# Kernel tuning notes

Hardware: AMD Instinct MI355X
Metric: run time of the kernel (lower is better)

## Reference

```python
import jax, jax.numpy as jnp
import numpy as np


def setup_inputs() -> dict:
    key = jax.random.key(0)
    k1, k2 = jax.random.split(key)
    B, N, M, C = 32, 4096, 4096, 3
    xyz1 = jax.random.normal(k1, (B, N, C), dtype=jnp.float32)
    xyz2 = jax.random.normal(k2, (B, M, C), dtype=jnp.float32)
    return {"xyz1": xyz1, "xyz2": xyz2}


def _chamfer_l2(xyz1, xyz2):
    # Pairwise squared L2 distances via ||a||^2 + ||b||^2 - 2 a.b  (b n m)
    sq1 = jnp.sum(xyz1 * xyz1, axis=-1)            # [B, N]
    sq2 = jnp.sum(xyz2 * xyz2, axis=-1)            # [B, M]
    cross = jnp.einsum('bnc,bmc->bnm', xyz1, xyz2) # [B, N, M]
    d = sq1[:, :, None] + sq2[:, None, :] - 2.0 * cross
    dist1 = jnp.min(d, axis=2)                     # [B, N] nearest in xyz2
    dist2 = jnp.min(d, axis=1)                     # [B, M] nearest in xyz1
    return jnp.mean(dist1, axis=-1) + jnp.mean(dist2, axis=-1)  # [B]


def reference(xyz1, xyz2):
    return _chamfer_l2(xyz1, xyz2)
```

## Files before the change

kernel.cpp:

```cpp
#include <hip/hip_runtime.h>

typedef _Float16 half8 __attribute__((ext_vector_type(8)));
typedef float floatx16 __attribute__((ext_vector_type(16)));

#define TPB   256
#define RPTS  1024
#define NTILE (RPTS / 32)
#define SMH   (RPTS * 16)

__device__ __forceinline__ unsigned enc(float f) {
    int b = __float_as_int(f);
    return (b >= 0) ? ((unsigned)b | 0x80000000u) : ~(unsigned)b;
}
__device__ __forceinline__ float dec(unsigned k) {
    int b = (k & 0x80000000u) ? (int)(k & 0x7FFFFFFFu) : (int)~k;
    return __int_as_float(b);
}

__global__ __launch_bounds__(256) void pack_frags(const float* __restrict__ src,
                                                  _Float16* __restrict__ dst,
                                                  int npts, int npad) {
    const int b = blockIdx.y;
    const int p = blockIdx.x * 256 + (int)threadIdx.x;
    if (p >= npad) return;
    const int g = p < npts ? p : npts - 1;
    const float* sp = src + ((size_t)b * npts + g) * 3;
    float x = sp[0], y = sp[1], z = sp[2];
    float hq = 0.5f * (x * x + y * y + z * z);
    _Float16 xh = (_Float16)x, yh = (_Float16)y, zh = (_Float16)z;
    _Float16 xl = (_Float16)(x - (float)xh);
    _Float16 yl = (_Float16)(y - (float)yh);
    _Float16 zl = (_Float16)(z - (float)zh);
    _Float16 qh = (_Float16)hq;
    _Float16 ql = (_Float16)(hq - (float)qh);
    const _Float16 hz = (_Float16)0.0f;
    half8 v0, v1;
    v0[0] = xh; v0[1] = xl; v0[2] = xh; v0[3] = yh;
    v0[4] = yl; v0[5] = yh; v0[6] = zh; v0[7] = zl;
    v1[0] = zh; v1[1] = qh; v1[2] = ql; v1[3] = hz;
    v1[4] = hz; v1[5] = hz; v1[6] = hz; v1[7] = hz;
    int t = p >> 5, c = p & 31;
    _Float16* base = dst + (size_t)b * npad * 16 + (size_t)t * 512 + c * 8;
    *(half8*)base         = v0;
    *(half8*)(base + 256) = v1;
}

__global__ __launch_bounds__(TPB, 4) void chamfer_ws(const float* __restrict__ xyz1,
                                                     const float* __restrict__ xyz2,
                                                     const _Float16* __restrict__ frag1,
                                                     const _Float16* __restrict__ frag2,
                                                     unsigned* __restrict__ dist,
                                                     int N, int M, int B,
                                                     int p1pad, int p2pad, int qpad) {
    const int b = blockIdx.y, dir = blockIdx.z;
    const float*    __restrict__ P = dir ? xyz2 + (size_t)b * M * 3 : xyz1 + (size_t)b * N * 3;
    const _Float16* __restrict__ F = dir ? frag1 + (size_t)b * p1pad * 16
                                         : frag2 + (size_t)b * p2pad * 16;
    const int nq    = dir ? M : N;
    const int mdpad = dir ? p1pad : p2pad;

    const int qblk = blockIdx.x >> 1;
    const int s    = blockIdx.x & 1;
    if (qblk * 256 >= nq) return;

    __shared__ __align__(16) _Float16 smB[SMH];

    const int tid = (int)threadIdx.x;
    const int w   = tid >> 6;
    const int l   = tid & 63;
    const int m   = l & 31;
    const int h   = l >> 5;

    const _Float16 hz = (_Float16)0.0f, hone = (_Float16)1.0f;
    const int qb = qblk * 256 + w * 64;

    half8 afr[2];
#pragma unroll
    for (int g = 0; g < 2; ++g) {
        int idx = qb + g * 32 + m;
        int ci  = idx < nq ? idx : nq - 1;
        float x = P[3 * ci], y = P[3 * ci + 1], z = P[3 * ci + 2];
        _Float16 xh = (_Float16)x, yh = (_Float16)y, zh = (_Float16)z;
        _Float16 xl = (_Float16)(x - (float)xh);
        _Float16 yl = (_Float16)(y - (float)yh);
        _Float16 zl = (_Float16)(z - (float)zh);
        half8 a;
        if (h == 0) {
            a[0] = -xh; a[1] = -xh; a[2] = -xl; a[3] = -yh;
            a[4] = -yh; a[5] = -yl; a[6] = -zh; a[7] = -zh;
        } else {
            a[0] = -zl; a[1] = hone; a[2] = hone; a[3] = hz;
            a[4] = hz;  a[5] = hz;   a[6] = hz;  a[7] = hz;
        }
        afr[g] = a;
    }

    float rm[32];
#pragma unroll
    for (int i = 0; i < 32; ++i) rm[i] = 3.0e38f;

    const floatx16 czero = {0.0f, 0.0f, 0.0f, 0.0f, 0.0f, 0.0f, 0.0f, 0.0f,
                            0.0f, 0.0f, 0.0f, 0.0f, 0.0f, 0.0f, 0.0f, 0.0f};
    const int nrounds = mdpad / RPTS;
    const _Float16* bp = smB + h * 256 + m * 8;

    for (int r = s; r < nrounds; r += 2) {
        if (r != s) __syncthreads();
        const int4* __restrict__ gsrc = (const int4*)(F + (size_t)r * SMH);
        int4* __restrict__ ldst = (int4*)smB;
#pragma unroll
        for (int k = 0; k < (SMH * 2 / 16) / TPB; ++k) {
            int c = k * TPB + tid;
            ldst[c] = gsrc[c];
        }
        __syncthreads();

        for (int t = 0; t < NTILE; t += 2) {
            half8 b0 = *(const half8*)(bp + t * 512);
            half8 b1 = *(const half8*)(bp + t * 512 + 512);
            floatx16 d0a = __builtin_amdgcn_mfma_f32_32x32x16_f16(afr[0], b0, czero, 0, 0, 0);
            floatx16 d0b = __builtin_amdgcn_mfma_f32_32x32x16_f16(afr[0], b1, czero, 0, 0, 0);
#pragma unroll
            for (int i = 0; i < 16; ++i)
                rm[i] = fminf(fminf(rm[i], d0a[i]), d0b[i]);
            floatx16 d1a = __builtin_amdgcn_mfma_f32_32x32x16_f16(afr[1], b0, czero, 0, 0, 0);
            floatx16 d1b = __builtin_amdgcn_mfma_f32_32x32x16_f16(afr[1], b1, czero, 0, 0, 0);
#pragma unroll
            for (int i = 0; i < 16; ++i)
                rm[16 + i] = fminf(fminf(rm[16 + i], d1a[i]), d1b[i]);
        }
    }

#pragma unroll
    for (int off = 1; off < 32; off <<= 1) {
#pragma unroll
        for (int i = 0; i < 32; ++i) rm[i] = fminf(rm[i], __shfl_xor(rm[i], off, 64));
    }

    unsigned* dptr = dist + (size_t)(dir * B + b) * qpad;
    if (m < 16) {
        const int reg = (m & 3) + 4 * (m >> 2);
        const int row = 4 * h + (m & 3) + 8 * (m >> 2);
#pragma unroll
        for (int g = 0; g < 2; ++g) {
            int idx = qb + g * 32 + row;
            if (idx < nq) {
                float x = P[3 * idx], y = P[3 * idx + 1], z = P[3 * idx + 2];
                float v = rm[g * 16 + reg] + 0.5f * (x * x + y * y + z * z);
                atomicMin(dptr + idx, enc(v));
            }
        }
    }
}

__global__ __launch_bounds__(256) void reduce_out(const unsigned* __restrict__ dist,
                                                  float* __restrict__ out,
                                                  int N, int M, int B, int qpad) {
    const int b = blockIdx.x;
    const int tid = (int)threadIdx.x;
    float s = 0.0f;
    const unsigned* d0 = dist + (size_t)b * qpad;
    const unsigned* d1 = dist + (size_t)(B + b) * qpad;
    for (int i = tid; i < N; i += 256) s += dec(d0[i]) * (1.0f / (float)N);
    for (int i = tid; i < M; i += 256) s += dec(d1[i]) * (1.0f / (float)M);
#pragma unroll
    for (int off = 32; off > 0; off >>= 1) s += __shfl_down(s, off, 64);
    __shared__ float red[4];
    if ((tid & 63) == 0) red[tid >> 6] = s;
    __syncthreads();
    if (tid == 0) out[b] = 2.0f * (red[0] + red[1] + red[2] + red[3]);
}

__global__ __launch_bounds__(TPB, 4) void chamfer_plain(const float* __restrict__ xyz1,
                                                        const float* __restrict__ xyz2,
                                                        float* __restrict__ out,
                                                        int N, int M) {
    const int b = blockIdx.y, dir = blockIdx.z;
    const float* __restrict__ P = dir ? xyz2 + (size_t)b * M * 3 : xyz1 + (size_t)b * N * 3;
    const float* __restrict__ Q = dir ? xyz1 + (size_t)b * N * 3 : xyz2 + (size_t)b * M * 3;
    const int nq = dir ? M : N;
    const int md = dir ? N : M;
    if ((int)blockIdx.x * TPB >= nq) return;
    __shared__ __align__(16) _Float16 smB[SMH];
    const int tid = (int)threadIdx.x;
    const int w = tid >> 6, l = tid & 63, m = l & 31, h = l >> 5;
    const _Float16 hz = (_Float16)0.0f, hone = (_Float16)1.0f;
    const int qb = blockIdx.x * 256 + w * 64;
    half8 afr[2];
#pragma unroll
    for (int g = 0; g < 2; ++g) {
        int idx = qb + g * 32 + m;
        int ci  = idx < nq ? idx : nq - 1;
        float x = P[3 * ci], y = P[3 * ci + 1], z = P[3 * ci + 2];
        _Float16 xh = (_Float16)x, yh = (_Float16)y, zh = (_Float16)z;
        _Float16 xl = (_Float16)(x - (float)xh);
        _Float16 yl = (_Float16)(y - (float)yh);
        _Float16 zl = (_Float16)(z - (float)zh);
        half8 a;
        if (h == 0) { a[0]=-xh;a[1]=-xh;a[2]=-xl;a[3]=-yh;a[4]=-yh;a[5]=-yl;a[6]=-zh;a[7]=-zh; }
        else        { a[0]=-zl;a[1]=hone;a[2]=hone;a[3]=hz;a[4]=hz;a[5]=hz;a[6]=hz;a[7]=hz; }
        afr[g] = a;
    }
    float rm[32];
#pragma unroll
    for (int i = 0; i < 32; ++i) rm[i] = 3.0e38f;
    const floatx16 czero = {0,0,0,0,0,0,0,0,0,0,0,0,0,0,0,0};
    const int nrounds = (md + RPTS - 1) / RPTS;
    const _Float16* bp = smB + h * 256 + m * 8;
    for (int r = 0; r < nrounds; ++r) {
        if (r) __syncthreads();
#pragma unroll
        for (int k = 0; k < RPTS / TPB; ++k) {
            int j = tid + k * TPB;
            int g = r * RPTS + j;
            g = g < md ? g : md - 1;
            float x = Q[3 * g], y = Q[3 * g + 1], z = Q[3 * g + 2];
            float hq = 0.5f * (x * x + y * y + z * z);
            _Float16 xh = (_Float16)x, yh = (_Float16)y, zh = (_Float16)z;
            _Float16 xl = (_Float16)(x - (float)xh);
            _Float16 yl = (_Float16)(y - (float)yh);
            _Float16 zl = (_Float16)(z - (float)zh);
            _Float16 qh = (_Float16)hq;
            _Float16 ql = (_Float16)(hq - (float)qh);
            int t = j >> 5, c = j & 31;
            half8 v0, v1;
            v0[0]=xh;v0[1]=xl;v0[2]=xh;v0[3]=yh;v0[4]=yl;v0[5]=yh;v0[6]=zh;v0[7]=zl;
            v1[0]=zh;v1[1]=qh;v1[2]=ql;v1[3]=hz;v1[4]=hz;v1[5]=hz;v1[6]=hz;v1[7]=hz;
            *(half8*)&smB[t * 512 + c * 8]       = v0;
            *(half8*)&smB[t * 512 + 256 + c * 8] = v1;
        }
        __syncthreads();
        for (int t = 0; t < NTILE; t += 2) {
            half8 b0 = *(const half8*)(bp + t * 512);
            half8 b1 = *(const half8*)(bp + t * 512 + 512);
            floatx16 d0a = __builtin_amdgcn_mfma_f32_32x32x16_f16(afr[0], b0, czero, 0, 0, 0);
            floatx16 d0b = __builtin_amdgcn_mfma_f32_32x32x16_f16(afr[0], b1, czero, 0, 0, 0);
#pragma unroll
            for (int i = 0; i < 16; ++i) rm[i] = fminf(fminf(rm[i], d0a[i]), d0b[i]);
            floatx16 d1a = __builtin_amdgcn_mfma_f32_32x32x16_f16(afr[1], b0, czero, 0, 0, 0);
            floatx16 d1b = __builtin_amdgcn_mfma_f32_32x32x16_f16(afr[1], b1, czero, 0, 0, 0);
#pragma unroll
            for (int i = 0; i < 16; ++i) rm[16+i] = fminf(fminf(rm[16+i], d1a[i]), d1b[i]);
        }
    }
#pragma unroll
    for (int off = 1; off < 32; off <<= 1) {
#pragma unroll
        for (int i = 0; i < 32; ++i) rm[i] = fminf(rm[i], __shfl_xor(rm[i], off, 64));
    }
    float s = 0.0f;
    if (m < 16) {
        const int reg = (m & 3) + 4 * (m >> 2);
        const int row = 4 * h + (m & 3) + 8 * (m >> 2);
#pragma unroll
        for (int g = 0; g < 2; ++g) {
            int idx = qb + g * 32 + row;
            if (idx < nq) {
                float x = P[3 * idx], y = P[3 * idx + 1], z = P[3 * idx + 2];
                s += rm[g * 16 + reg] + 0.5f * (x * x + y * y + z * z);
            }
        }
    }
#pragma unroll
    for (int off = 32; off > 0; off >>= 1) s += __shfl_down(s, off, 64);
    if (l == 0) atomicAdd(out + b, s * (2.0f / (float)nq));
}

extern "C" void kernel_launch(void* const* d_in, const int* in_sizes, int n_in,
                              void* d_out, int out_size, void* d_ws, size_t ws_size,
                              hipStream_t stream) {
    const float* xyz1 = (const float*)d_in[0];
    const float* xyz2 = (const float*)d_in[1];
    float* out = (float*)d_out;

    const int B = out_size;
    const int N = in_sizes[0] / (3 * B);
    const int M = in_sizes[1] / (3 * B);
    const int qmax = N > M ? N : M;

    const int p1pad = ((N + RPTS - 1) / RPTS) * RPTS;
    const int p2pad = ((M + RPTS - 1) / RPTS) * RPTS;
    const int qpad  = p1pad > p2pad ? p1pad : p2pad;
    const size_t f1bytes = (size_t)B * p1pad * 32;
    const size_t f2bytes = (size_t)B * p2pad * 32;
    const size_t dbytes  = (size_t)2 * B * qpad * sizeof(unsigned);

    if (ws_size >= f1bytes + f2bytes + dbytes) {
        _Float16* frag1 = (_Float16*)d_ws;
        _Float16* frag2 = (_Float16*)((char*)d_ws + f1bytes);
        unsigned* dist  = (unsigned*)((char*)d_ws + f1bytes + f2bytes);

        pack_frags<<<dim3(p1pad / 256, B), dim3(256), 0, stream>>>(xyz1, frag1, N, p1pad);
        pack_frags<<<dim3(p2pad / 256, B), dim3(256), 0, stream>>>(xyz2, frag2, M, p2pad);
        hipMemsetAsync(dist, 0xFF, dbytes, stream);

        dim3 grid(((qmax + 255) / 256) * 2, B, 2);
        chamfer_ws<<<grid, dim3(TPB), 0, stream>>>(xyz1, xyz2, frag1, frag2, dist,
                                                   N, M, B, p1pad, p2pad, qpad);
        reduce_out<<<dim3(B), dim3(256), 0, stream>>>(dist, out, N, M, B, qpad);
    } else {
        hipMemsetAsync(out, 0, (size_t)B * sizeof(float), stream);
        dim3 grid((qmax + 255) / 256, B, 2);
        chamfer_plain<<<grid, dim3(TPB), 0, stream>>>(xyz1, xyz2, out, N, M);
    }
}
```

Baseline: 117.9 us.

## Fuse pack/memset launches, split query work four ways, software-pipeline MFMA min loop

Merges the two pack kernels and the distance memset into one launch that also zeros the output, removing several launch overheads. Raises the work split over reference rounds from 2 to 4 blocks per query tile, giving more blocks and parallelism but more atomic-min traffic and fewer rounds per block. Software-pipelines the MFMA loop so the next tile's matrix products are issued before the previous results are min-reduced, hiding MFMA latency at the cost of extra registers. The final reduce now accumulates into the output instead of overwriting it.

```diff
diff --git a/kernel.cpp b/kernel.cpp
--- a/kernel.cpp
+++ b/kernel.cpp
@@ -7,6 +7,7 @@
 #define RPTS  1024
 #define NTILE (RPTS / 32)
 #define SMH   (RPTS * 16)
+#define SPLIT 4
 
 __device__ __forceinline__ unsigned enc(float f) {
     int b = __float_as_int(f);
@@ -17,20 +18,37 @@
     return __int_as_float(b);
 }
 
-__global__ __launch_bounds__(256) void pack_frags(const float* __restrict__ src,
-                                                  _Float16* __restrict__ dst,
-                                                  int npts, int npad) {
+__global__ __launch_bounds__(256) void pack_all(const float* __restrict__ xyz1,
+                                                const float* __restrict__ xyz2,
+                                                _Float16* __restrict__ frag1,
+                                                _Float16* __restrict__ frag2,
+                                                unsigned* __restrict__ dist,
+                                                float* __restrict__ out,
+                                                int N, int M, int B,
+                                                int p1pad, int p2pad, int qpad) {
     const int b = blockIdx.y;
+    const int z = blockIdx.z;
     const int p = blockIdx.x * 256 + (int)threadIdx.x;
+
+    if (z == 0 && b == 0 && blockIdx.x == 0) {
+        for (int i = (int)threadIdx.x; i < B; i += 256) out[i] = 0.0f;
+    }
+    if (p < qpad) dist[(size_t)(z * B + b) * qpad + p] = 0xFFFFFFFFu;
+
+    const int   npts = z ? M : N;
+    const int   npad = z ? p2pad : p1pad;
     if (p >= npad) return;
+    const float* src = z ? xyz2 : xyz1;
+    _Float16*    dst = z ? frag2 : frag1;
+
     const int g = p < npts ? p : npts - 1;
     const float* sp = src + ((size_t)b * npts + g) * 3;
-    float x = sp[0], y = sp[1], z = sp[2];
-    float hq = 0.5f * (x * x + y * y + z * z);
-    _Float16 xh = (_Float16)x, yh = (_Float16)y, zh = (_Float16)z;
+    float x = sp[0], y = sp[1], zc = sp[2];
+    float hq = 0.5f * (x * x + y * y + zc * zc);
+    _Float16 xh = (_Float16)x, yh = (_Float16)y, zh = (_Float16)zc;
     _Float16 xl = (_Float16)(x - (float)xh);
     _Float16 yl = (_Float16)(y - (float)yh);
-    _Float16 zl = (_Float16)(z - (float)zh);
+    _Float16 zl = (_Float16)(zc - (float)zh);
     _Float16 qh = (_Float16)hq;
     _Float16 ql = (_Float16)(hq - (float)qh);
     const _Float16 hz = (_Float16)0.0f;
@@ -59,8 +77,8 @@
     const int nq    = dir ? M : N;
     const int mdpad = dir ? p1pad : p2pad;
 
-    const int qblk = blockIdx.x >> 1;
-    const int s    = blockIdx.x & 1;
+    const int qblk = blockIdx.x / SPLIT;
+    const int s    = blockIdx.x % SPLIT;
     if (qblk * 256 >= nq) return;
 
     __shared__ __align__(16) _Float16 smB[SMH];
@@ -104,7 +122,7 @@
     const int nrounds = mdpad / RPTS;
     const _Float16* bp = smB + h * 256 + m * 8;
 
-    for (int r = s; r < nrounds; r += 2) {
+    for (int r = s; r < nrounds; r += SPLIT) {
         if (r != s) __syncthreads();
         const int4* __restrict__ gsrc = (const int4*)(F + (size_t)r * SMH);
         int4* __restrict__ ldst = (int4*)smB;
@@ -115,19 +133,30 @@
         }
         __syncthreads();
 
-        for (int t = 0; t < NTILE; t += 2) {
-            half8 b0 = *(const half8*)(bp + t * 512);
-            half8 b1 = *(const half8*)(bp + t * 512 + 512);
-            floatx16 d0a = __builtin_amdgcn_mfma_f32_32x32x16_f16(afr[0], b0, czero, 0, 0, 0);
-            floatx16 d0b = __builtin_amdgcn_mfma_f32_32x32x16_f16(afr[0], b1, czero, 0, 0, 0);
-#pragma unroll
-            for (int i = 0; i < 16; ++i)
-                rm[i] = fminf(fminf(rm[i], d0a[i]), d0b[i]);
-            floatx16 d1a = __builtin_amdgcn_mfma_f32_32x32x16_f16(afr[1], b0, czero, 0, 0, 0);
-            floatx16 d1b = __builtin_amdgcn_mfma_f32_32x32x16_f16(afr[1], b1, czero, 0, 0, 0);
-#pragma unroll
-            for (int i = 0; i < 16; ++i)
-                rm[16 + i] = fminf(fminf(rm[16 + i], d1a[i]), d1b[i]);
+        half8 c0 = *(const half8*)(bp);
+        half8 c1 = *(const half8*)(bp + 512);
+        floatx16 p0a = __builtin_amdgcn_mfma_f32_32x32x16_f16(afr[0], c0, czero, 0, 0, 0);
+        floatx16 p0b = __builtin_amdgcn_mfma_f32_32x32x16_f16(afr[0], c1, czero, 0, 0, 0);
+        floatx16 p1a = __builtin_amdgcn_mfma_f32_32x32x16_f16(afr[1], c0, czero, 0, 0, 0);
+        floatx16 p1b = __builtin_amdgcn_mfma_f32_32x32x16_f16(afr[1], c1, czero, 0, 0, 0);
+        for (int t = 2; t < NTILE; t += 2) {
+            half8 n0 = *(const half8*)(bp + t * 512);
+            half8 n1 = *(const half8*)(bp + t * 512 + 512);
+            floatx16 q0a = __builtin_amdgcn_mfma_f32_32x32x16_f16(afr[0], n0, czero, 0, 0, 0);
+            floatx16 q0b = __builtin_amdgcn_mfma_f32_32x32x16_f16(afr[0], n1, czero, 0, 0, 0);
+            floatx16 q1a = __builtin_amdgcn_mfma_f32_32x32x16_f16(afr[1], n0, czero, 0, 0, 0);
+            floatx16 q1b = __builtin_amdgcn_mfma_f32_32x32x16_f16(afr[1], n1, czero, 0, 0, 0);
+#pragma unroll
+            for (int i = 0; i < 16; ++i) {
+                rm[i]      = fminf(fminf(rm[i],      p0a[i]), p0b[i]);
+                rm[16 + i] = fminf(fminf(rm[16 + i], p1a[i]), p1b[i]);
+            }
+            p0a = q0a; p0b = q0b; p1a = q1a; p1b = q1b;
+        }
+#pragma unroll
+        for (int i = 0; i < 16; ++i) {
+            rm[i]      = fminf(fminf(rm[i],      p0a[i]), p0b[i]);
+            rm[16 + i] = fminf(fminf(rm[16 + i], p1a[i]), p1b[i]);
         }
     }
 
@@ -168,7 +197,7 @@
     __shared__ float red[4];
     if ((tid & 63) == 0) red[tid >> 6] = s;
     __syncthreads();
-    if (tid == 0) out[b] = 2.0f * (red[0] + red[1] + red[2] + red[3]);
+    if (tid == 0) out[b] += 2.0f * (red[0] + red[1] + red[2] + red[3]);
 }
 
 __global__ __launch_bounds__(TPB, 4) void chamfer_plain(const float* __restrict__ xyz1,
@@ -290,11 +319,10 @@
         _Float16* frag2 = (_Float16*)((char*)d_ws + f1bytes);
         unsigned* dist  = (unsigned*)((char*)d_ws + f1bytes + f2bytes);
 
-        pack_frags<<<dim3(p1pad / 256, B), dim3(256), 0, stream>>>(xyz1, frag1, N, p1pad);
-        pack_frags<<<dim3(p2pad / 256, B), dim3(256), 0, stream>>>(xyz2, frag2, M, p2pad);
-        hipMemsetAsync(dist, 0xFF, dbytes, stream);
-
-        dim3 grid(((qmax + 255) / 256) * 2, B, 2);
+        pack_all<<<dim3(qpad / 256, B, 2), dim3(256), 0, stream>>>(
+            xyz1, xyz2, frag1, frag2, dist, out, N, M, B, p1pad, p2pad, qpad);
+
+        dim3 grid(((qmax + 255) / 256) * SPLIT, B, 2);
         chamfer_ws<<<grid, dim3(TPB), 0, stream>>>(xyz1, xyz2, frag1, frag2, dist,
                                                    N, M, B, p1pad, p2pad, qpad);
         reduce_out<<<dim3(B), dim3(256), 0, stream>>>(dist, out, N, M, B, qpad);
```

New measurement: 131.0 us. 11.1% more time.
